# Optimization experiments

Measured on AMD Instinct MI355X. Metric: run time of the kernel, lower is better.

## Reference

```python
import jax, jax.numpy as jnp
import numpy as np

NH, NL, NP = 8, 4, 4  # heads, levels, points per head per level
SHAPES = [(100, 134), (50, 67), (25, 34), (13, 17)]  # (H, W) per level, strides 8/16/32/64


def rms_norm(x, w, eps=1e-6):
    return x * jax.lax.rsqrt(jnp.mean(x * x, axis=-1, keepdims=True) + eps) * w


def bilinear_sample(value_l, loc, H, W):
    """grid_sample(bilinear, zeros padding, align_corners=False) equivalent.
    value_l: (bs, nh, H*W, d); loc: (bs, Lq, nh, P, 2) normalized to [0,1].
    Returns (bs, Lq, nh, P, d)."""
    bs, Lq, nh, P, _ = loc.shape
    x = loc[..., 0] * W - 0.5
    y = loc[..., 1] * H - 0.5
    x0 = jnp.floor(x); y0 = jnp.floor(y)
    lx = x - x0; ly = y - y0
    x0i = x0.astype(jnp.int32); y0i = y0.astype(jnp.int32)
    out = None
    for dy, dx in ((0, 0), (0, 1), (1, 0), (1, 1)):
        wgt = (lx if dx else 1.0 - lx) * (ly if dy else 1.0 - ly)
        xi = x0i + dx; yi = y0i + dy
        valid = (xi >= 0) & (xi < W) & (yi >= 0) & (yi < H)
        idx = jnp.clip(yi, 0, H - 1) * W + jnp.clip(xi, 0, W - 1)  # (bs,Lq,nh,P)
        idx_t = idx.transpose(0, 2, 1, 3).reshape(bs, nh, Lq * P)
        g = jnp.take_along_axis(value_l, idx_t[..., None], axis=2)  # (bs,nh,Lq*P,d)
        g = g.reshape(bs, nh, Lq, P, -1).transpose(0, 2, 1, 3, 4)    # (bs,Lq,nh,P,d)
        term = g * (wgt * valid)[..., None]
        out = term if out is None else out + term
    return out


def _forward(query, query_pos, reference_points, norm_attn_w, Wv, bv, Woff, boff, Waw, baw, Wo, bo, ls_attn_g, norm_ffn_w, W1, b1, W2, b2, W3, b3, ls_ffn_g):
    bs, Lq, C = query.shape
    d = C // NH
    # --- pre-norm MSDeformAttn with identity=0 (LayerScale residual applied outside) ---
    normed = rms_norm(query, norm_attn_w)
    q = normed + query_pos  # query_pos only affects offsets/weights, not value
    value = (normed @ Wv.T + bv).reshape(bs, Lq, NH, d).transpose(0, 2, 1, 3)  # (bs,nh,Nv,d)
    off = (q @ Woff.T + boff).reshape(bs, Lq, NH, NL, NP, 2)
    aw = jax.nn.softmax((q @ Waw.T + baw).reshape(bs, Lq, NH, NL * NP), axis=-1)
    aw = aw.reshape(bs, Lq, NH, NL, NP)
    normalizer = jnp.array([[w, h] for (h, w) in SHAPES], dtype=query.dtype)  # (NL,2) = (W,H)
    loc = reference_points[:, :, None, :, None, :] + off / normalizer[None, None, None, :, None, :]
    out = jnp.zeros((bs, Lq, NH, d), query.dtype)
    start = 0
    for l, (H, W) in enumerate(SHAPES):
        v_l = jax.lax.dynamic_slice_in_dim(value, start, H * W, axis=2)
        samp = bilinear_sample(v_l, loc[:, :, :, l], H, W)  # (bs,Lq,nh,P,d)
        out = out + jnp.einsum('bqhpd,bqhp->bqhd', samp, aw[:, :, :, l])
        start += H * W
    attn_out = out.reshape(bs, Lq, C) @ Wo.T + bo
    x = query + ls_attn_g * attn_out
    # --- pre-norm SwiGLU FFN with LayerScale residual ---
    n2 = rms_norm(x, norm_ffn_w)
    h = jax.nn.silu(n2 @ W1.T + b1) * (n2 @ W2.T + b2)
    return x + ls_ffn_g * (h @ W3.T + b3)


def setup_inputs() -> dict:
    key = jax.random.key(0)
    ks = jax.random.split(key, 12)
    bs, C, dffn = 2, 256, 1024
    Lq = sum(h * w for h, w in SHAPES)  # 17821
    p = 0.02
    return {
        'query': jax.random.normal(ks[0], (bs, Lq, C), jnp.float32),
        'query_pos': jax.random.normal(ks[1], (bs, Lq, C), jnp.float32),
        'reference_points': jax.random.uniform(ks[2], (bs, Lq, NL, 2), jnp.float32),
        'spatial_shapes': jnp.array(SHAPES, jnp.int32),
        'level_start_index': jnp.array(np.cumsum([0] + [h * w for h, w in SHAPES])[:-1], jnp.int32),
        'norm_attn_w': jnp.ones((C,), jnp.float32),
        'Wv': jax.random.normal(ks[3], (C, C), jnp.float32) * p,
        'bv': jnp.zeros((C,), jnp.float32),
        'Woff': jax.random.normal(ks[4], (NH * NL * NP * 2, C), jnp.float32) * p,
        'boff': jax.random.uniform(ks[5], (NH * NL * NP * 2,), jnp.float32, -1.0, 1.0),
        'Waw': jax.random.normal(ks[6], (NH * NL * NP, C), jnp.float32) * p,
        'baw': jnp.zeros((NH * NL * NP,), jnp.float32),
        'Wo': jax.random.normal(ks[7], (C, C), jnp.float32) * p,
        'bo': jnp.zeros((C,), jnp.float32),
        'ls_attn_g': jnp.full((C,), 1e-4, jnp.float32),
        'norm_ffn_w': jnp.ones((C,), jnp.float32),
        'W1': jax.random.normal(ks[8], (dffn, C), jnp.float32) * p,
        'b1': jnp.zeros((dffn,), jnp.float32),
        'W2': jax.random.normal(ks[9], (dffn, C), jnp.float32) * p,
        'b2': jnp.zeros((dffn,), jnp.float32),
        'W3': jax.random.normal(ks[10], (C, dffn), jnp.float32) * p,
        'b3': jnp.zeros((C,), jnp.float32),
        'ls_ffn_g': jnp.full((C,), 1e-4, jnp.float32),
    }


def reference(query, query_pos, reference_points, spatial_shapes, level_start_index, norm_attn_w, Wv, bv, Woff, boff, Waw, baw, Wo, bo, ls_attn_g, norm_ffn_w, W1, b1, W2, b2, W3, b3, ls_ffn_g):
    del spatial_shapes, level_start_index  # static shapes baked into SHAPES
    return _forward(query, query_pos, reference_points, norm_attn_w, Wv, bv, Woff, boff, Waw, baw, Wo, bo, ls_attn_g, norm_ffn_w, W1, b1, W2, b2, W3, b3, ls_ffn_g)
```

## Files before the change

kernel.cpp:

```cpp
#include <hip/hip_runtime.h>
#include <hip/hip_bf16.h>
#include <cstddef>

#define LQ   17821
#define BS   2
#define MTOK (BS * LQ)
#define CDIM 256
#define NHD  8
#define DHEAD 32
#define DFFN 1024

typedef short bf16x4 __attribute__((ext_vector_type(4)));
typedef short bf16x8 __attribute__((ext_vector_type(8)));
typedef float f32x4  __attribute__((ext_vector_type(4)));
typedef float f32x2  __attribute__((ext_vector_type(2)));

__device__ __forceinline__ unsigned char fp8_enc(float f) {
#if __has_builtin(__builtin_amdgcn_cvt_pk_fp8_f32)
    return (unsigned char)(__builtin_amdgcn_cvt_pk_fp8_f32(f, f, 0, false) & 0xff);
#else
    unsigned s = (__float_as_uint(f) >> 31) << 7;
    float af = fabsf(f);
    if (af < 0.0078125f) return (unsigned char)s;
    af = fminf(af, 448.f);
    unsigned b = __float_as_uint(af);
    int e = (int)(b >> 23) - 127 + 7;
    unsigned m = (b >> 20) & 7;
    if (b & 0x80000) { m++; if (m == 8) { m = 0; e++; } }
    if (e < 1) return (unsigned char)s;
    if (e > 15) { e = 15; m = 6; }
    return (unsigned char)(s | ((unsigned)e << 3) | m);
#endif
}

__device__ __forceinline__ float fp8_dec_byte(unsigned x) {
    unsigned s = (x >> 7) & 1, e = (x >> 3) & 15, m = x & 7;
    float v = e ? __uint_as_float(((e + 120u) << 23) | (m << 20))
                : (float)m * 0.001953125f;
    return s ? -v : v;
}

template <bool HI>
__device__ __forceinline__ f32x2 fp8_dec2(unsigned d) {
#if __has_builtin(__builtin_amdgcn_cvt_pk_f32_fp8)
    return __builtin_amdgcn_cvt_pk_f32_fp8(d, HI);
#else
    f32x2 r;
    r[0] = fp8_dec_byte((d >> (HI ? 16 : 0)) & 0xff);
    r[1] = fp8_dec_byte((d >> (HI ? 24 : 8)) & 0xff);
    return r;
#endif
}

__device__ __forceinline__ ushort bfpack(float f) {
    __hip_bfloat16 h = (__hip_bfloat16)f;
    return *(ushort*)&h;
}

__device__ __forceinline__ void stage_a8(short* p, uint2 d) {
    const f32x2 p0 = fp8_dec2<false>(d.x), p1 = fp8_dec2<true>(d.x);
    const f32x2 p2 = fp8_dec2<false>(d.y), p3 = fp8_dec2<true>(d.y);
    bf16x4 lo, hi;
    lo[0] = (short)bfpack(p0[0]); lo[1] = (short)bfpack(p0[1]);
    lo[2] = (short)bfpack(p1[0]); lo[3] = (short)bfpack(p1[1]);
    hi[0] = (short)bfpack(p2[0]); hi[1] = (short)bfpack(p2[1]);
    hi[2] = (short)bfpack(p3[0]); hi[3] = (short)bfpack(p3[1]);
    ((bf16x4*)p)[0] = lo;
    ((bf16x4*)p)[1] = hi;
}

struct CastJobs {
    const float* src[7];
    __hip_bfloat16* dst[7];
    const float* colw[7];
    int n[7];
};

__global__ __launch_bounds__(256)
void cast_all(CastJobs j) {
    const int seg = blockIdx.y;
    const int i = blockIdx.x * 256 + threadIdx.x;
    if (i < j.n[seg]) {
        float v = j.src[seg][i];
        if (j.colw[seg]) v *= j.colw[seg][i & 255];
        j.dst[seg][i] = (__hip_bfloat16)v;
    }
}

template <bool ADD_POS>
__global__ __launch_bounds__(256)
void rmsnorm_kernel(const float* __restrict__ x, const float* __restrict__ pos,
                    const float* __restrict__ w,
                    __hip_bfloat16* __restrict__ outN, __hip_bfloat16* __restrict__ outQ) {
    const int tok = blockIdx.x * 4 + (threadIdx.x >> 6);
    if (tok >= MTOK) return;
    const int lane = threadIdx.x & 63;
    const size_t base = (size_t)tok * CDIM + lane * 4;
    const float4 v = *(const float4*)&x[base];
    float ss = v.x * v.x + v.y * v.y + v.z * v.z + v.w * v.w;
#pragma unroll
    for (int m = 1; m < 64; m <<= 1) ss += __shfl_xor(ss, m, 64);
    const float r = rsqrtf(ss * (1.0f / CDIM) + 1e-6f);
    const float4 wv = *(const float4*)&w[lane * 4];
    const float n0 = v.x * r * wv.x, n1 = v.y * r * wv.y;
    const float n2 = v.z * r * wv.z, n3 = v.w * r * wv.w;
    ushort4 o;
    o.x = bfpack(n0); o.y = bfpack(n1); o.z = bfpack(n2); o.w = bfpack(n3);
    *(ushort4*)&outN[base] = o;
    if (ADD_POS) {
        const float4 p = *(const float4*)&pos[base];
        ushort4 q;
        q.x = bfpack(n0 + p.x); q.y = bfpack(n1 + p.y);
        q.z = bfpack(n2 + p.z); q.w = bfpack(n3 + p.w);
        *(ushort4*)&outQ[base] = q;
    }
}

__global__ __launch_bounds__(256)
void rowrms_kernel(const __hip_bfloat16* __restrict__ x, float* __restrict__ r) {
    const int tok = blockIdx.x * 4 + (threadIdx.x >> 6);
    if (tok >= MTOK) return;
    const int lane = threadIdx.x & 63;
    const ushort4 u = *(const ushort4*)&x[(size_t)tok * CDIM + lane * 4];
    const float v0 = __uint_as_float((unsigned)u.x << 16);
    const float v1 = __uint_as_float((unsigned)u.y << 16);
    const float v2 = __uint_as_float((unsigned)u.z << 16);
    const float v3 = __uint_as_float((unsigned)u.w << 16);
    float ss = v0 * v0 + v1 * v1 + v2 * v2 + v3 * v3;
#pragma unroll
    for (int m = 1; m < 64; m <<= 1) ss += __shfl_xor(ss, m, 64);
    if (lane == 0) r[tok] = rsqrtf(ss * (1.0f / CDIM) + 1e-6f);
}

#define GBM 128
#define GBN 128

template <int MODE, int BKT, typename OUTT, bool A8 = false>
__global__ __launch_bounds__(256, 2)
void mfma_gemm(const void* __restrict__ Av,
               const __hip_bfloat16* __restrict__ B1, const float* __restrict__ bias1,
               const float* __restrict__ bias2,
               const float* __restrict__ resid, const __hip_bfloat16* __restrict__ residb,
               const float* __restrict__ ls,
               OUTT* __restrict__ out, int M, int N, int K, int nsw) {
    constexpr int LDKT = BKT + 8;
    constexpr int CH = BKT / 16;
    constexpr int CPR = BKT / 8;

    __shared__ short As[GBM * LDKT];
    __shared__ short Bs[GBN * LDKT];

    const __hip_bfloat16* A = (const __hip_bfloat16*)Av;
    const unsigned char* A8p = (const unsigned char*)Av;

    const int tid = threadIdx.x;
    const int bid = blockIdx.x;
    const int m0 = (bid / nsw) * GBM;
    const int n0 = (bid % nsw) * GBN;
    const int wave = tid >> 6;
    const int lane = tid & 63;
    const int wm = (wave >> 1) * 64;
    const int wn = (wave & 1) * 64;
    const int fr = lane & 15;
    const int fq = lane >> 4;

    f32x4 acc[4][4] = {};

    int srow[CH], skc[CH];
#pragma unroll
    for (int cc = 0; cc < CH; ++cc) {
        const int g = tid + cc * 256;
        srow[cc] = g / CPR;
        skc[cc] = (g % CPR) * 8;
    }
    const uint4 zero4 = make_uint4(0, 0, 0, 0);
    const uint2 zero2 = make_uint2(0, 0);

    uint4 ra[CH], rb[CH];
    uint2 ra8[A8 ? CH : 1];
#pragma unroll
    for (int cc = 0; cc < CH; ++cc) {
        const int gm = m0 + srow[cc];
        if constexpr (A8)
            ra8[cc] = (gm < M) ? *(const uint2*)&A8p[(size_t)gm * K + skc[cc]] : zero2;
        else
            ra[cc] = (gm < M) ? *(const uint4*)&A[(size_t)gm * K + skc[cc]] : zero4;
        rb[cc] = *(const uint4*)&B1[(size_t)(n0 + srow[cc]) * K + skc[cc]];
    }

    for (int k0 = 0; k0 < K; k0 += BKT) {
        __syncthreads();
#pragma unroll
        for (int cc = 0; cc < CH; ++cc) {
            short* pa = &As[srow[cc] * LDKT + skc[cc]];
            short* pb = &Bs[srow[cc] * LDKT + skc[cc]];
            if constexpr (A8) {
                stage_a8(pa, ra8[cc]);
            } else {
                union { uint4 u; bf16x4 h[2]; } cv;
                cv.u = ra[cc]; ((bf16x4*)pa)[0] = cv.h[0]; ((bf16x4*)pa)[1] = cv.h[1];
            }
            union { uint4 u; bf16x4 h[2]; } cv;
            cv.u = rb[cc]; ((bf16x4*)pb)[0] = cv.h[0]; ((bf16x4*)pb)[1] = cv.h[1];
        }
        __syncthreads();

        if (k0 + BKT < K) {
            const int kn = k0 + BKT;
#pragma unroll
            for (int cc = 0; cc < CH; ++cc) {
                const int gm = m0 + srow[cc];
                if constexpr (A8)
                    ra8[cc] = (gm < M) ? *(const uint2*)&A8p[(size_t)gm * K + kn + skc[cc]] : zero2;
                else
                    ra[cc] = (gm < M) ? *(const uint4*)&A[(size_t)gm * K + kn + skc[cc]] : zero4;
                rb[cc] = *(const uint4*)&B1[(size_t)(n0 + srow[cc]) * K + kn + skc[cc]];
            }
        }

#pragma unroll
        for (int kk = 0; kk < BKT; kk += 32) {
            const int kq = kk + fq * 8;
            bf16x8 af[4], bfr[4];
#pragma unroll
            for (int i = 0; i < 4; ++i)
                af[i] = *(const bf16x8*)&As[(wm + i * 16 + fr) * LDKT + kq];
#pragma unroll
            for (int j = 0; j < 4; ++j)
                bfr[j] = *(const bf16x8*)&Bs[(wn + j * 16 + fr) * LDKT + kq];
#pragma unroll
            for (int i = 0; i < 4; ++i)
#pragma unroll
                for (int j = 0; j < 4; ++j)
                    acc[i][j] = __builtin_amdgcn_mfma_f32_16x16x32_bf16(af[i], bfr[j], acc[i][j], 0, 0, 0);
        }
    }

#pragma unroll
    for (int i = 0; i < 4; ++i) {
#pragma unroll
        for (int r = 0; r < 4; ++r) {
            const int m = m0 + wm + i * 16 + fq * 4 + r;
            if (m >= M) continue;
#pragma unroll
            for (int j = 0; j < 4; ++j) {
                const int n = n0 + wn + j * 16 + fr;
                float v;
                if constexpr (MODE == 4)
                    v = acc[i][j][r] + ((n < 256) ? bias1[n] : bias2[n - 256]);
                else
                    v = acc[i][j][r] + bias1[n];
                if constexpr (MODE == 0 || MODE == 4) {
                    out[(size_t)m * N + n] = (OUTT)v;
                } else if constexpr (MODE == 1) {
                    const int b = (m >= LQ) ? 1 : 0;
                    const int qi = m - b * LQ;
                    const int h = n >> 5;
                    const int c = n & 31;
                    ((unsigned char*)out)[((size_t)(b * NHD + h) * LQ + qi) * DHEAD + c] = fp8_enc(v);
                } else if constexpr (MODE == 2) {
                    out[(size_t)m * N + n] =
                        (OUTT)(resid[(size_t)m * N + n] + ls[n] * v);
                } else {
                    const float rx = __uint_as_float(
                        (unsigned)(*(const ushort*)&residb[(size_t)m * N + n]) << 16);
                    out[(size_t)m * N + n] = (OUTT)(rx + ls[n] * v);
                }
            }
        }
    }
}

__global__ __launch_bounds__(256, 3)
void mfma_swiglu(const __hip_bfloat16* __restrict__ A,
                 const __hip_bfloat16* __restrict__ B1, const float* __restrict__ bias1,
                 const __hip_bfloat16* __restrict__ B2, const float* __restrict__ bias2,
                 const float* __restrict__ rrow,
                 unsigned char* __restrict__ out, int M) {
    constexpr int BKT = 32, LDKT = 40, K = CDIM, N = DFFN;
    __shared__ short As[128 * LDKT];
    __shared__ short Bs[64 * LDKT];
    __shared__ short Bs2[64 * LDKT];

    const int tid = threadIdx.x;
    const int bid = blockIdx.x;
    const int m0 = (bid >> 4) * 128;
    const int n0 = (bid & 15) * 64;
    const int wave = tid >> 6;
    const int lane = tid & 63;
    const int wm = (wave >> 1) * 64;
    const int wn = (wave & 1) * 32;
    const int fr = lane & 15;
    const int fq = lane >> 4;

    f32x4 acc[4][2] = {};
    f32x4 acc2[4][2] = {};

    const int arow = tid >> 2;
    const int akc = (tid & 3) * 8;
    const uint4 zero4 = make_uint4(0, 0, 0, 0);

    uint4 ra0, ra1, rb, rc;
    {
        const int gm0 = m0 + arow, gm1 = m0 + arow + 64;
        ra0 = (gm0 < M) ? *(const uint4*)&A[(size_t)gm0 * K + akc] : zero4;
        ra1 = (gm1 < M) ? *(const uint4*)&A[(size_t)gm1 * K + akc] : zero4;
        rb = *(const uint4*)&B1[(size_t)(n0 + arow) * K + akc];
        rc = *(const uint4*)&B2[(size_t)(n0 + arow) * K + akc];
    }

    for (int k0 = 0; k0 < K; k0 += BKT) {
        __syncthreads();
        {
            union { uint4 u; bf16x4 h[2]; } cv;
            short* pa0 = &As[arow * LDKT + akc];
            short* pa1 = &As[(arow + 64) * LDKT + akc];
            short* pb = &Bs[arow * LDKT + akc];
            short* pc = &Bs2[arow * LDKT + akc];
            cv.u = ra0; ((bf16x4*)pa0)[0] = cv.h[0]; ((bf16x4*)pa0)[1] = cv.h[1];
            cv.u = ra1; ((bf16x4*)pa1)[0] = cv.h[0]; ((bf16x4*)pa1)[1] = cv.h[1];
            cv.u = rb;  ((bf16x4*)pb)[0] = cv.h[0]; ((bf16x4*)pb)[1] = cv.h[1];
            cv.u = rc;  ((bf16x4*)pc)[0] = cv.h[0]; ((bf16x4*)pc)[1] = cv.h[1];
        }
        __syncthreads();

        if (k0 + BKT < K) {
            const int kn = k0 + BKT + akc;
            const int gm0 = m0 + arow, gm1 = m0 + arow + 64;
            ra0 = (gm0 < M) ? *(const uint4*)&A[(size_t)gm0 * K + kn] : zero4;
            ra1 = (gm1 < M) ? *(const uint4*)&A[(size_t)gm1 * K + kn] : zero4;
            rb = *(const uint4*)&B1[(size_t)(n0 + arow) * K + kn];
            rc = *(const uint4*)&B2[(size_t)(n0 + arow) * K + kn];
        }

        const int kq = fq * 8;
        bf16x8 af[4], bfr[2], bg[2];
#pragma unroll
        for (int i = 0; i < 4; ++i)
            af[i] = *(const bf16x8*)&As[(wm + i * 16 + fr) * LDKT + kq];
#pragma unroll
        for (int j = 0; j < 2; ++j) {
            bfr[j] = *(const bf16x8*)&Bs[(wn + j * 16 + fr) * LDKT + kq];
            bg[j] = *(const bf16x8*)&Bs2[(wn + j * 16 + fr) * LDKT + kq];
        }
#pragma unroll
        for (int i = 0; i < 4; ++i)
#pragma unroll
            for (int j = 0; j < 2; ++j) {
                acc[i][j] = __builtin_amdgcn_mfma_f32_16x16x32_bf16(af[i], bfr[j], acc[i][j], 0, 0, 0);
                acc2[i][j] = __builtin_amdgcn_mfma_f32_16x16x32_bf16(af[i], bg[j], acc2[i][j], 0, 0, 0);
            }
    }

#pragma unroll
    for (int i = 0; i < 4; ++i) {
#pragma unroll
        for (int r = 0; r < 4; ++r) {
            const int m = m0 + wm + i * 16 + fq * 4 + r;
            if (m >= M) continue;
            const float rm = rrow[m];
#pragma unroll
            for (int j = 0; j < 2; ++j) {
                const int n = n0 + wn + j * 16 + fr;
                const float v1 = acc[i][j][r] * rm + bias1[n];
                const float v2 = acc2[i][j][r] * rm + bias2[n];
                const float sig = 1.0f / (1.0f + __expf(-v1));
                out[(size_t)m * N + n] = fp8_enc(v1 * sig * v2);
            }
        }
    }
}

__global__ __launch_bounds__(256)
void sample_kernel(const unsigned char* __restrict__ value,
                   const ushort* __restrict__ proj,
                   const float* __restrict__ ref,
                   __hip_bfloat16* __restrict__ out) {
    __shared__ float wsm[4][NHD][16];
    __shared__ int2  sTap[4][64][9];

    const int tok0 = blockIdx.x * 4;
    const int t = threadIdx.x;

    if (t < 32) {
        const int tl = t >> 3, h = t & 7;
        const int row = tok0 + tl;
        if (row < MTOK) {
            const ushort* lg = &proj[(size_t)row * 384 + 256 + h * 16];
            float v[16];
            float mx = -3.4e38f;
#pragma unroll
            for (int i = 0; i < 16; ++i) {
                v[i] = __uint_as_float((unsigned)lg[i] << 16);
                mx = fmaxf(mx, v[i]);
            }
            float s = 0.f;
#pragma unroll
            for (int i = 0; i < 16; ++i) { v[i] = __expf(v[i] - mx); s += v[i]; }
            const float inv = 1.0f / s;
#pragma unroll
            for (int i = 0; i < 16; ++i) wsm[tl][h][i] = v[i] * inv;
        }
    }
    __syncthreads();

#pragma unroll
    for (int e = t; e < 512; e += 256) {
        const int tl = e >> 7, hp = e & 127;
        const int row = tok0 + tl;
        if (row < MTOK) {
            const int h = hp >> 4, pt = hp & 15, lv = pt >> 2;
            const int Hs[4] = {100, 50, 25, 13};
            const int Ws[4] = {134, 67, 34, 17};
            const int stt[4] = {0, 13400, 16750, 17600};
            const int H = Hs[lv], W = Ws[lv];
            const float rx = ref[((size_t)row * 4 + lv) * 2 + 0];
            const float ry = ref[((size_t)row * 4 + lv) * 2 + 1];
            const float ox = __uint_as_float((unsigned)proj[(size_t)row * 384 + h * 32 + pt * 2 + 0] << 16);
            const float oy = __uint_as_float((unsigned)proj[(size_t)row * 384 + h * 32 + pt * 2 + 1] << 16);
            const float xf = rx * (float)W + ox - 0.5f;
            const float yf = ry * (float)H + oy - 0.5f;
            const float x0f = floorf(xf), y0f = floorf(yf);
            const float fx = xf - x0f, fy = yf - y0f;
            const int x0 = (int)x0f, y0 = (int)y0f;
            const float aw = wsm[tl][h][pt];
            const int b = (row >= LQ) ? 1 : 0;
            const int base = (b * NHD + h) * LQ + stt[lv];
#pragma unroll
            for (int tap = 0; tap < 4; ++tap) {
                const int dy = tap >> 1, dx = tap & 1;
                const int xi = x0 + dx, yi = y0 + dy;
                const bool valid = (xi >= 0) & (xi < W) & (yi >= 0) & (yi < H);
                const float wgt = (dx ? fx : 1.f - fx) * (dy ? fy : 1.f - fy) * aw;
                sTap[tl][pt * 4 + tap][h] = valid
                    ? make_int2((base + yi * W + xi) * DHEAD, __float_as_int(wgt))
                    : make_int2(0, 0);
            }
        }
    }
    __syncthreads();

    const int tl = t >> 6, lane = t & 63;
    const int row = tok0 + tl;
    if (row >= MTOK) return;
    const int h = lane >> 3, c0 = (lane & 7) * 4;
    const unsigned char* vb = value + c0;
    float a0 = 0.f, a1 = 0.f, a2 = 0.f, a3 = 0.f;
#pragma unroll 8
    for (int i = 0; i < 64; ++i) {
        const int2 tp = sTap[tl][i][h];
        const float w = __int_as_float(tp.y);
        const unsigned d = *(const unsigned*)(vb + (size_t)tp.x);
        const f32x2 lo = fp8_dec2<false>(d);
        const f32x2 hi = fp8_dec2<true>(d);
        a0 = fmaf(w, lo[0], a0);
        a1 = fmaf(w, lo[1], a1);
        a2 = fmaf(w, hi[0], a2);
        a3 = fmaf(w, hi[1], a3);
    }
    ushort4 o;
    o.x = bfpack(a0); o.y = bfpack(a1); o.z = bfpack(a2); o.w = bfpack(a3);
    *(ushort4*)&out[(size_t)row * 256 + h * 32 + c0] = o;
}

extern "C" void kernel_launch(void* const* d_in, const int* in_sizes, int n_in,
                              void* d_out, int out_size, void* d_ws, size_t ws_size,
                              hipStream_t stream) {
    const float* query      = (const float*)d_in[0];
    const float* query_pos  = (const float*)d_in[1];
    const float* ref        = (const float*)d_in[2];
    const float* norm_attn_w = (const float*)d_in[5];
    const float* Wv   = (const float*)d_in[6];
    const float* bv   = (const float*)d_in[7];
    const float* Woff = (const float*)d_in[8];
    const float* boff = (const float*)d_in[9];
    const float* Waw  = (const float*)d_in[10];
    const float* baw  = (const float*)d_in[11];
    const float* Wo   = (const float*)d_in[12];
    const float* bo   = (const float*)d_in[13];
    const float* ls_attn = (const float*)d_in[14];
    const float* norm_ffn_w = (const float*)d_in[15];
    const float* W1 = (const float*)d_in[16];
    const float* b1 = (const float*)d_in[17];
    const float* W2 = (const float*)d_in[18];
    const float* b2 = (const float*)d_in[19];
    const float* W3 = (const float*)d_in[20];
    const float* b3 = (const float*)d_in[21];
    const float* ls_ffn = (const float*)d_in[22];
    float* out = (float*)d_out;

    char* ws = (char*)d_ws;
    const size_t MCb = (size_t)MTOK * CDIM * 2;

    __hip_bfloat16* normed_bf  = (__hip_bfloat16*)(ws);
    __hip_bfloat16* q_bf       = (__hip_bfloat16*)(ws + MCb);
    unsigned char*  value_u8   = (unsigned char*)(ws + 2 * MCb);
    __hip_bfloat16* proj_bf    = (__hip_bfloat16*)(ws + 3 * MCb);
    __hip_bfloat16* sampled_bf = (__hip_bfloat16*)(ws);
    __hip_bfloat16* x_bf       = (__hip_bfloat16*)(ws + MCb);
    float*          r_f        = (float*)(ws + 2 * MCb);
    unsigned char*  h_u8       = (unsigned char*)(ws + 3 * MCb);
    __hip_bfloat16* wbf        = (__hip_bfloat16*)(ws + 7 * MCb);

    __hip_bfloat16* Wv_bf    = wbf;
    __hip_bfloat16* Wproj_bf = wbf + 65536;
    __hip_bfloat16* Wo_bf    = wbf + 163840;
    __hip_bfloat16* W1_bf    = wbf + 229376;
    __hip_bfloat16* W2_bf    = wbf + 491520;
    __hip_bfloat16* W3_bf    = wbf + 753664;

    CastJobs cj;
    cj.src[0] = Wv;   cj.dst[0] = Wv_bf;            cj.colw[0] = nullptr; cj.n[0] = 65536;
    cj.src[1] = Woff; cj.dst[1] = Wproj_bf;         cj.colw[1] = nullptr; cj.n[1] = 65536;
    cj.src[2] = Waw;  cj.dst[2] = Wproj_bf + 65536; cj.colw[2] = nullptr; cj.n[2] = 32768;
    cj.src[3] = Wo;   cj.dst[3] = Wo_bf;            cj.colw[3] = nullptr; cj.n[3] = 65536;
    cj.src[4] = W1;   cj.dst[4] = W1_bf;            cj.colw[4] = norm_ffn_w; cj.n[4] = 262144;
    cj.src[5] = W2;   cj.dst[5] = W2_bf;            cj.colw[5] = norm_ffn_w; cj.n[5] = 262144;
    cj.src[6] = W3;   cj.dst[6] = W3_bf;            cj.colw[6] = nullptr; cj.n[6] = 262144;
    cast_all<<<dim3(1024, 7), 256, 0, stream>>>(cj);

    const int gx = (MTOK + GBM - 1) / GBM;
    const int gr = (MTOK + 3) / 4;

    rmsnorm_kernel<true><<<gr, 256, 0, stream>>>(query, query_pos, norm_attn_w, normed_bf, q_bf);
    mfma_gemm<1, 64, unsigned char><<<gx * 2, 256, 0, stream>>>(
        normed_bf, Wv_bf, bv, nullptr, nullptr, nullptr, nullptr, value_u8, MTOK, CDIM, CDIM, 2);
    mfma_gemm<4, 64, __hip_bfloat16><<<gx * 3, 256, 0, stream>>>(
        q_bf, Wproj_bf, boff, baw, nullptr, nullptr, nullptr, proj_bf, MTOK, 384, CDIM, 3);
    sample_kernel<<<gr, 256, 0, stream>>>(value_u8, (const ushort*)proj_bf, ref, sampled_bf);
    mfma_gemm<2, 64, __hip_bfloat16><<<gx * 2, 256, 0, stream>>>(
        sampled_bf, Wo_bf, bo, nullptr, query, nullptr, ls_attn, x_bf, MTOK, CDIM, CDIM, 2);
    rowrms_kernel<<<gr, 256, 0, stream>>>(x_bf, r_f);
    mfma_swiglu<<<gx * 16, 256, 0, stream>>>(
        x_bf, W1_bf, b1, W2_bf, b2, r_f, h_u8, MTOK);
    mfma_gemm<5, 64, float, true><<<gx * 2, 256, 0, stream>>>(
        h_u8, W3_bf, b3, nullptr, nullptr, x_bf, ls_ffn, out, MTOK, CDIM, DFFN, 2);
}
```

Measured before the change: 380.0 us.

## Load SwiGLU GEMM tiles directly into LDS with XOR-swizzled layout

Replaces the register-staged global-to-LDS copy in the SwiGLU GEMM with direct global_load_lds 16-byte transfers. The tile is stored in an XOR-swizzled LDS layout to avoid bank conflicts, and BK grows from 32 to 64, halving the number of K iterations and barriers. This drops the register round-trip and the padded layout, but it loses the software prefetch overlap: loads are now issued and waited on within the same iteration. Out-of-range rows are clamped to M-1 instead of being zeroed.

Measured after the change: 377.7 us. No clear change (-0.6%).

```diff
diff --git a/kernel.cpp b/kernel.cpp
--- a/kernel.cpp
+++ b/kernel.cpp
@@ -14,6 +14,13 @@
 typedef short bf16x8 __attribute__((ext_vector_type(8)));
 typedef float f32x4  __attribute__((ext_vector_type(4)));
 typedef float f32x2  __attribute__((ext_vector_type(2)));
+
+typedef const __attribute__((address_space(1))) unsigned char gcu8;
+typedef __attribute__((address_space(3))) unsigned char lu8;
+
+__device__ __forceinline__ void gload16(const void* g, void* l) {
+    __builtin_amdgcn_global_load_lds((gcu8*)g, (lu8*)l, 16, 0, 0);
+}
 
 __device__ __forceinline__ unsigned char fp8_enc(float f) {
 #if __has_builtin(__builtin_amdgcn_cvt_pk_fp8_f32)
@@ -277,10 +284,10 @@
                  const __hip_bfloat16* __restrict__ B2, const float* __restrict__ bias2,
                  const float* __restrict__ rrow,
                  unsigned char* __restrict__ out, int M) {
-    constexpr int BKT = 32, LDKT = 40, K = CDIM, N = DFFN;
-    __shared__ short As[128 * LDKT];
-    __shared__ short Bs[64 * LDKT];
-    __shared__ short Bs2[64 * LDKT];
+    constexpr int BKT = 64, K = CDIM, N = DFFN;
+    __shared__ short As[128 * 64];
+    __shared__ short Bs[64 * 64];
+    __shared__ short Bs2[64 * 64];
 
     const int tid = threadIdx.x;
     const int bid = blockIdx.x;
@@ -296,60 +303,54 @@
     f32x4 acc[4][2] = {};
     f32x4 acc2[4][2] = {};
 
-    const int arow = tid >> 2;
-    const int akc = (tid & 3) * 8;
-    const uint4 zero4 = make_uint4(0, 0, 0, 0);
-
-    uint4 ra0, ra1, rb, rc;
-    {
-        const int gm0 = m0 + arow, gm1 = m0 + arow + 64;
-        ra0 = (gm0 < M) ? *(const uint4*)&A[(size_t)gm0 * K + akc] : zero4;
-        ra1 = (gm1 < M) ? *(const uint4*)&A[(size_t)gm1 * K + akc] : zero4;
-        rb = *(const uint4*)&B1[(size_t)(n0 + arow) * K + akc];
-        rc = *(const uint4*)&B2[(size_t)(n0 + arow) * K + akc];
-    }
+    const int lrow = lane >> 3;
+    const int lcol = (lane & 7) ^ lrow;
+    const char* Ab  = (const char*)A;
+    const char* B1b = (const char*)B1;
+    const char* B2b = (const char*)B2;
+    char* AsB  = (char*)As;
+    char* BsB  = (char*)Bs;
+    char* Bs2B = (char*)Bs2;
 
     for (int k0 = 0; k0 < K; k0 += BKT) {
         __syncthreads();
-        {
-            union { uint4 u; bf16x4 h[2]; } cv;
-            short* pa0 = &As[arow * LDKT + akc];
-            short* pa1 = &As[(arow + 64) * LDKT + akc];
-            short* pb = &Bs[arow * LDKT + akc];
-            short* pc = &Bs2[arow * LDKT + akc];
-            cv.u = ra0; ((bf16x4*)pa0)[0] = cv.h[0]; ((bf16x4*)pa0)[1] = cv.h[1];
-            cv.u = ra1; ((bf16x4*)pa1)[0] = cv.h[0]; ((bf16x4*)pa1)[1] = cv.h[1];
-            cv.u = rb;  ((bf16x4*)pb)[0] = cv.h[0]; ((bf16x4*)pb)[1] = cv.h[1];
-            cv.u = rc;  ((bf16x4*)pc)[0] = cv.h[0]; ((bf16x4*)pc)[1] = cv.h[1];
+#pragma unroll
+        for (int q = 0; q < 4; ++q) {
+            const int c = wave * 4 + q;
+            int gm = m0 + c * 8 + lrow;
+            gm = (gm < M) ? gm : (M - 1);
+            gload16(Ab + ((size_t)gm * K + k0) * 2 + lcol * 16, AsB + c * 1024);
+        }
+#pragma unroll
+        for (int q = 0; q < 2; ++q) {
+            const int c = wave * 2 + q;
+            const size_t rn = (size_t)(n0 + c * 8 + lrow) * K + k0;
+            gload16(B1b + rn * 2 + lcol * 16, BsB + c * 1024);
+            gload16(B2b + rn * 2 + lcol * 16, Bs2B + c * 1024);
         }
         __syncthreads();
 
-        if (k0 + BKT < K) {
-            const int kn = k0 + BKT + akc;
-            const int gm0 = m0 + arow, gm1 = m0 + arow + 64;
-            ra0 = (gm0 < M) ? *(const uint4*)&A[(size_t)gm0 * K + kn] : zero4;
-            ra1 = (gm1 < M) ? *(const uint4*)&A[(size_t)gm1 * K + kn] : zero4;
-            rb = *(const uint4*)&B1[(size_t)(n0 + arow) * K + kn];
-            rc = *(const uint4*)&B2[(size_t)(n0 + arow) * K + kn];
-        }
-
-        const int kq = fq * 8;
-        bf16x8 af[4], bfr[2], bg[2];
-#pragma unroll
-        for (int i = 0; i < 4; ++i)
-            af[i] = *(const bf16x8*)&As[(wm + i * 16 + fr) * LDKT + kq];
-#pragma unroll
-        for (int j = 0; j < 2; ++j) {
-            bfr[j] = *(const bf16x8*)&Bs[(wn + j * 16 + fr) * LDKT + kq];
-            bg[j] = *(const bf16x8*)&Bs2[(wn + j * 16 + fr) * LDKT + kq];
-        }
-#pragma unroll
-        for (int i = 0; i < 4; ++i)
+        const int swz = (fr & 7) << 4;
+#pragma unroll
+        for (int kk = 0; kk < BKT; kk += 32) {
+            const int co = ((kk * 2 + fq * 16) ^ swz) >> 1;
+            bf16x8 af[4], bfr[2], bg[2];
+#pragma unroll
+            for (int i = 0; i < 4; ++i)
+                af[i] = *(const bf16x8*)&As[(wm + i * 16 + fr) * 64 + co];
 #pragma unroll
             for (int j = 0; j < 2; ++j) {
-                acc[i][j] = __builtin_amdgcn_mfma_f32_16x16x32_bf16(af[i], bfr[j], acc[i][j], 0, 0, 0);
-                acc2[i][j] = __builtin_amdgcn_mfma_f32_16x16x32_bf16(af[i], bg[j], acc2[i][j], 0, 0, 0);
-            }
+                bfr[j] = *(const bf16x8*)&Bs[(wn + j * 16 + fr) * 64 + co];
+                bg[j] = *(const bf16x8*)&Bs2[(wn + j * 16 + fr) * 64 + co];
+            }
+#pragma unroll
+            for (int i = 0; i < 4; ++i)
+#pragma unroll
+                for (int j = 0; j < 2; ++j) {
+                    acc[i][j] = __builtin_amdgcn_mfma_f32_16x16x32_bf16(af[i], bfr[j], acc[i][j], 0, 0, 0);
+                    acc2[i][j] = __builtin_amdgcn_mfma_f32_16x16x32_bf16(af[i], bg[j], acc2[i][j], 0, 0, 0);
+                }
+        }
     }
 
 #pragma unroll
```
